# Optimization experiments

Measured on AMD Instinct MI355X. Metric: run time of the kernel, lower is better.

## Reference

```python
import jax, jax.numpy as jnp
import numpy as np

NC, L, C, V, H = 4, 3, 32, 512, 512
B, T, N = 32, 64, 8

def setup_inputs() -> dict:
    key = jax.random.key(0)
    ks = jax.random.split(key, 12)
    inp = {
        "x": jax.random.normal(ks[0], (B, T, N, H), dtype=jnp.float32),
        "comms": jax.random.randint(ks[1], (B, T, N, NC, L), 0, V, dtype=jnp.int64),
        "codebook": jax.random.normal(ks[2], (L, V, C), dtype=jnp.float32),
    }
    for l in range(L):
        fan_in = H + l * NC * C
        inp[f"W{l}"] = jax.random.normal(ks[3 + 2 * l], (NC * V, fan_in), dtype=jnp.float32) / np.sqrt(fan_in)
        inp[f"b{l}"] = jax.random.normal(ks[4 + 2 * l], (NC * V,), dtype=jnp.float32) * 0.01
    return inp


def reference(x, comms, codebook, W0, b0, W1, b1, W2, b2):
    # x: [B,T,N,H]; comms: [B,T,N,NC,L] int indices; codebook: [L,V,C]
    Bs, Ts, Ns, _ = x.shape
    params = [(W0, b0), (W1, b1), (W2, b2)]
    cond = x
    log_probs = jnp.zeros((Bs, Ts, Ns), dtype=x.dtype)
    entropy = jnp.zeros((Bs, Ts, Ns), dtype=x.dtype)
    hard_levels, soft_levels = [], []
    for l in range(L):
        W, b = params[l]
        logits = (cond @ W.T + b).reshape(Bs, Ts, Ns, NC, V)
        logp = jax.nn.log_softmax(logits, axis=-1)
        p = jnp.exp(logp)
        idx = comms[..., l]  # [B,T,N,NC]
        # log-prob of chosen codes, summed over comm channels
        lp = jnp.take_along_axis(logp, idx[..., None], axis=-1)[..., 0]
        log_probs = log_probs + lp.sum(axis=-1)
        # categorical entropy, summed over comm channels
        entropy = entropy + (-(p * logp).sum(axis=-1)).sum(axis=-1)
        hard = codebook[l][idx]                               # [B,T,N,NC,C]
        soft = jnp.einsum('btnkv,vc->btnkc', p, codebook[l])  # [B,T,N,NC,C]
        hard_levels.append(hard)
        soft_levels.append(soft)
        cond = jnp.concatenate([cond, hard.reshape(Bs, Ts, Ns, NC * C)], axis=-1)
    hard_s = jnp.stack(hard_levels, axis=-2)  # [B,T,N,NC,L,C]
    soft_s = jnp.stack(soft_levels, axis=-2)
    # straight-through estimator
    codewords = soft_s + jax.lax.stop_gradient(hard_s - soft_s)
    comm_output = codewords.sum(axis=-2).reshape(-1, NC * C)  # sum over hq levels
    return comm_output, log_probs, entropy
```

## Files before the change

kernel.cpp:

```cpp
#include <hip/hip_runtime.h>
#include <hip/hip_bf16.h>

#define NCC 4
#define LL 3
#define CCC 32
#define VVV 512
#define HHH 512
#define ROWS_TOTAL 16384
#define CONDW 768

typedef float f32x4 __attribute__((ext_vector_type(4)));
typedef long  i64f;
typedef long  i64x2 __attribute__((ext_vector_type(2)));

__device__ __forceinline__ void gload_lds16(const void* g, void* l) {
    __builtin_amdgcn_global_load_lds(
        (const __attribute__((address_space(1))) void*)g,
        (__attribute__((address_space(3))) void*)l, 16, 0, 0);
}

__device__ __forceinline__ int pk4_fp8(float a, float b, float c, float d) {
    int w = __builtin_amdgcn_cvt_pk_fp8_f32(a, b, 0, false);
    w = __builtin_amdgcn_cvt_pk_fp8_f32(c, d, w, true);
    return w;
}

__device__ __forceinline__ int perm_off(int b) {
    return (b & ~63) | ((b & 0x18) << 1) | ((b & 0x20) >> 2) | (b & 7);
}

__global__ void convert_w_fp8(const float* __restrict__ src, unsigned char* __restrict__ dst, int n) {
    int i = (blockIdx.x * blockDim.x + threadIdx.x) * 8;
    if (i + 7 < n) {
        const float4 v0 = *reinterpret_cast<const float4*>(src + i);
        const float4 v1 = *reinterpret_cast<const float4*>(src + i + 4);
        int2 p;
        p.x = pk4_fp8(v0.x, v0.y, v0.z, v0.w);
        p.y = pk4_fp8(v1.x, v1.y, v1.z, v1.w);
        *reinterpret_cast<int2*>(dst + perm_off(i)) = p;
    }
}

__global__ void build_cond(const float* __restrict__ x,
                           const int* __restrict__ comms,
                           const float* __restrict__ codebook,
                           unsigned char* __restrict__ cond,
                           float* __restrict__ comm_out) {
    const int r = blockIdx.x;
    const int t = threadIdx.x;
    const float4 v = reinterpret_cast<const float4*>(x + (size_t)r * HHH)[t];
    unsigned char* crow = cond + (size_t)r * CONDW;
    *reinterpret_cast<int*>(crow + perm_off(t * 4)) = pk4_fp8(v.x, v.y, v.z, v.w);
    const int k = t >> 5, c = t & 31;
    float s = 0.f;
    #pragma unroll
    for (int l = 0; l < LL; ++l) {
        const int vi = comms[r * (NCC * LL) + k * LL + l];
        const float val = codebook[((size_t)(l * VVV + vi)) * CCC + c];
        s += val;
        if (l < 2)
            crow[perm_off(HHH + l * (NCC * CCC) + t)] =
                (unsigned char)(__builtin_amdgcn_cvt_pk_fp8_f32(val, val, 0, false) & 0xff);
    }
    comm_out[(size_t)r * (NCC * CCC) + t] = s;
}

__global__ __launch_bounds__(256, 4) void gemm_partials(
    const unsigned char* __restrict__ cond,
    const unsigned char* __restrict__ wq,
    const float* __restrict__ b0, const float* __restrict__ b1, const float* __restrict__ b2,
    const int* __restrict__ comms,
    float4* __restrict__ partials)
{
    const int rb  = blockIdx.x;
    const int y   = blockIdx.y;
    const int lvl = blockIdx.z;
    const int K = HHH + lvl * (NCC * CCC);
    const unsigned char* W =
        wq + (lvl == 0 ? 0 : (lvl == 1 ? 2048 * 512 : 2048 * 512 + 2048 * 640));
    const float* bias = (lvl == 0) ? b0 : (lvl == 1 ? b1 : b2);

    const int tid  = threadIdx.x;
    const int lane = tid & 63;
    const int w    = tid >> 6;
    const int wr   = w >> 1;
    const int wc   = w & 1;
    const int lc   = lane & 15;
    const int kq   = lane >> 4;
    const int rchunk = (kq ^ ((lc >> 1) & 3)) << 4;

    const int rowBase = rb * 128;
    const int colBase = y * 128;

    __shared__ __align__(16) char LDS[32768];

    const int sc = (lane & 3) ^ ((lane >> 3) & 3);
    const unsigned char* gA = cond + (size_t)(rowBase + w * 32 + (lane >> 2)) * CONDW + sc * 16;
    const unsigned char* gB = W    + (size_t)(colBase + w * 32 + (lane >> 2)) * K     + sc * 16;

#define STAGE(B, KS) do {                                              \
        char* ab = LDS + (B) * 16384 + w * 2048;                       \
        gload_lds16(gA + (KS), ab);                                    \
        gload_lds16(gA + (size_t)16 * CONDW + (KS), ab + 1024);        \
        gload_lds16(gB + (KS), ab + 8192);                             \
        gload_lds16(gB + (size_t)16 * K + (KS), ab + 8192 + 1024);     \
    } while (0)

    f32x4 acc[4][4] = {};

    const int NT = K >> 6;
    STAGE(0, 0);
    asm volatile("s_waitcnt vmcnt(0)" ::: "memory");
    __builtin_amdgcn_s_barrier();

    for (int t = 0; t < NT; ++t) {
        const int cur = t & 1;
        if (t + 1 < NT) STAGE(cur ^ 1, (t + 1) * 64);
        const char* Ab = LDS + cur * 16384;
        const char* Bb = Ab + 8192;
        i64x2 af[4], bf[4];
        #pragma unroll
        for (int m = 0; m < 4; ++m)
            af[m] = *reinterpret_cast<const i64x2*>(
                Ab + (wr * 64 + m * 16 + lc) * 64 + rchunk);
        #pragma unroll
        for (int n = 0; n < 4; ++n)
            bf[n] = *reinterpret_cast<const i64x2*>(
                Bb + (wc * 64 + n * 16 + lc) * 64 + rchunk);
        __builtin_amdgcn_s_setprio(1);
        #pragma unroll
        for (int m = 0; m < 4; ++m)
            #pragma unroll
            for (int n = 0; n < 4; ++n)
                acc[m][n] = __builtin_amdgcn_mfma_f32_16x16x32_fp8_fp8(
                    af[m][0], bf[n][0], acc[m][n], 0, 0, 0);
        #pragma unroll
        for (int m = 0; m < 4; ++m)
            #pragma unroll
            for (int n = 0; n < 4; ++n)
                acc[m][n] = __builtin_amdgcn_mfma_f32_16x16x32_fp8_fp8(
                    af[m][1], bf[n][1], acc[m][n], 0, 0, 0);
        __builtin_amdgcn_s_setprio(0);
        asm volatile("s_waitcnt vmcnt(0)" ::: "memory");
        __builtin_amdgcn_s_barrier();
    }
#undef STAGE

    float* redS  = (float*)LDS;
    float* redT  = redS + 256;
    float* redTL = redT + 256;

    const int g   = y >> 2;
    const int cig = y & 3;
    float bv[4];
    #pragma unroll
    for (int n = 0; n < 4; ++n) bv[n] = bias[colBase + wc * 64 + n * 16 + lc];

    #pragma unroll
    for (int m = 0; m < 4; ++m) {
        float sv[4] = {0, 0, 0, 0}, tv[4] = {0, 0, 0, 0};
        #pragma unroll
        for (int i = 0; i < 4; ++i) {
            #pragma unroll
            for (int n = 0; n < 4; ++n) {
                const float z = acc[m][n][i] + bv[n];
                const float e = __expf(z);
                sv[i] += e;
                tv[i] += e * z;
            }
            #pragma unroll
            for (int off = 1; off < 16; off <<= 1) {
                sv[i] += __shfl_xor(sv[i], off);
                tv[i] += __shfl_xor(tv[i], off);
            }
        }
        #pragma unroll
        for (int i = 0; i < 4; ++i) {
            const int rloc = wr * 64 + m * 16 + kq * 4 + i;
            const int tcol = comms[(size_t)(rowBase + rloc) * (NCC * LL) + g * LL + lvl];
            #pragma unroll
            for (int n = 0; n < 4; ++n) {
                const int colg = cig * 128 + wc * 64 + n * 16 + lc;
                if (colg == tcol) redTL[rloc] = acc[m][n][i] + bv[n];
            }
        }
        if (lc == 0) {
            #pragma unroll
            for (int i = 0; i < 4; ++i) {
                const int rloc = wr * 64 + m * 16 + kq * 4 + i;
                redS[wc * 128 + rloc] = sv[i];
                redT[wc * 128 + rloc] = tv[i];
            }
        }
    }
    __syncthreads();
    if (tid < 128) {
        const int r = tid;
        const float S = redS[r] + redS[128 + r];
        const float T = redT[r] + redT[128 + r];
        partials[((size_t)lvl * ROWS_TOTAL + rowBase + r) * 16 + y] =
            make_float4(0.f, S, T, redTL[r]);
    }
}

__global__ void combine(const float4* __restrict__ partials,
                        const int* __restrict__ comms,
                        float* __restrict__ lp_out, float* __restrict__ ent_out)
{
    const int row = blockIdx.x * 256 + threadIdx.x;
    if (row >= ROWS_TOTAL) return;
    float lp = 0.f, ent = 0.f;
    #pragma unroll
    for (int lvl = 0; lvl < LL; ++lvl) {
        const float4* base = partials + ((size_t)lvl * ROWS_TOTAL + row) * 16;
        #pragma unroll
        for (int g = 0; g < NCC; ++g) {
            const int tcol = comms[(size_t)row * (NCC * LL) + g * LL + lvl];
            float S = 0.f, T = 0.f, tl = 0.f;
            #pragma unroll
            for (int k = 0; k < 4; ++k) {
                const float4 c = base[g * 4 + k];
                S += c.y;
                T += c.z;
                if ((tcol >> 7) == k) tl = c.w;
            }
            const float logZ = __logf(S);
            ent += logZ - T / S;
            lp += tl - logZ;
        }
    }
    lp_out[row] = lp;
    ent_out[row] = ent;
}

extern "C" void kernel_launch(void* const* d_in, const int* in_sizes, int n_in,
                              void* d_out, int out_size, void* d_ws, size_t ws_size,
                              hipStream_t stream) {
    const float* x        = (const float*)d_in[0];
    const int*   comms    = (const int*)d_in[1];
    const float* codebook = (const float*)d_in[2];
    const float* W0 = (const float*)d_in[3];
    const float* b0 = (const float*)d_in[4];
    const float* W1 = (const float*)d_in[5];
    const float* b1 = (const float*)d_in[6];
    const float* W2 = (const float*)d_in[7];
    const float* b2 = (const float*)d_in[8];

    float* out      = (float*)d_out;
    float* comm_out = out;
    float* lp_out   = out + (size_t)ROWS_TOTAL * 128;
    float* ent_out  = lp_out + ROWS_TOTAL;

    unsigned char* wq   = (unsigned char*)d_ws;
    unsigned char* cond = (unsigned char*)d_ws + 7864320;
    float4*       parts = (float4*)((char*)d_ws + 7864320 + 12582912);

    const int n0 = 2048 * 512, n1 = 2048 * 640, n2 = 2048 * 768;
    convert_w_fp8<<<n0 / 8 / 256, 256, 0, stream>>>(W0, wq, n0);
    convert_w_fp8<<<n1 / 8 / 256, 256, 0, stream>>>(W1, wq + n0, n1);
    convert_w_fp8<<<n2 / 8 / 256, 256, 0, stream>>>(W2, wq + n0 + n1, n2);

    build_cond<<<ROWS_TOTAL, 128, 0, stream>>>(x, comms, codebook, cond, comm_out);

    dim3 grid(ROWS_TOTAL / 128, 16, LL);
    gemm_partials<<<grid, 256, 0, stream>>>(cond, wq, b0, b1, b2, comms, parts);

    combine<<<ROWS_TOTAL / 256, 256, 0, stream>>>(parts, comms, lp_out, ent_out);
}
```

Baseline: 152.9 us.

## Pre-pack FP8 weights into MFMA fragment order and load B directly to registers

The weight conversion kernel now writes FP8 weights in a layout that matches the per-lane MFMA B-fragment order. The GEMM then loads B fragments straight from global memory into registers instead of staging them through LDS. This halves the LDS footprint, which may allow higher occupancy, and removes the LDS writes and reads for B. The cost is that each wave issues global loads for B directly, with cross-block reuse left to the cache. The global-load latency also sits inside the loop, since B is no longer prefetched a stage ahead.

Measured after the change: 145.8 us. 4.7% less time.

```diff
diff --git a/kernel.cpp b/kernel.cpp
--- a/kernel.cpp
+++ b/kernel.cpp
@@ -10,7 +10,6 @@
 #define CONDW 768
 
 typedef float f32x4 __attribute__((ext_vector_type(4)));
-typedef long  i64f;
 typedef long  i64x2 __attribute__((ext_vector_type(2)));
 
 __device__ __forceinline__ void gload_lds16(const void* g, void* l) {
@@ -29,16 +28,20 @@
     return (b & ~63) | ((b & 0x18) << 1) | ((b & 0x20) >> 2) | (b & 7);
 }
 
-__global__ void convert_w_fp8(const float* __restrict__ src, unsigned char* __restrict__ dst, int n) {
-    int i = (blockIdx.x * blockDim.x + threadIdx.x) * 8;
-    if (i + 7 < n) {
-        const float4 v0 = *reinterpret_cast<const float4*>(src + i);
-        const float4 v1 = *reinterpret_cast<const float4*>(src + i + 4);
-        int2 p;
-        p.x = pk4_fp8(v0.x, v0.y, v0.z, v0.w);
-        p.y = pk4_fp8(v1.x, v1.y, v1.z, v1.w);
-        *reinterpret_cast<int2*>(dst + perm_off(i)) = p;
-    }
+__global__ void convert_w_pack(const float* __restrict__ src, unsigned char* __restrict__ dst, int K) {
+    const int j  = blockIdx.x * 256 + threadIdx.x;
+    const int kc = K >> 3;
+    const int r  = j / kc;
+    const int k0 = (j - r * kc) * 8;
+    const float4 v0 = *reinterpret_cast<const float4*>(src + (size_t)r * K + k0);
+    const float4 v1 = *reinterpret_cast<const float4*>(src + (size_t)r * K + k0 + 4);
+    int2 p;
+    p.x = pk4_fp8(v0.x, v0.y, v0.z, v0.w);
+    p.y = pk4_fp8(v1.x, v1.y, v1.z, v1.w);
+    const int ct = r >> 4, lc = r & 15;
+    const int t = k0 >> 6, s = (k0 >> 5) & 1, kq = (k0 >> 3) & 3;
+    const size_t off = ((size_t)((t * 128 + ct) * 64 + kq * 16 + lc)) * 16 + s * 8;
+    *reinterpret_cast<int2*>(dst + off) = p;
 }
 
 __global__ void build_cond(const float* __restrict__ x,
@@ -76,7 +79,7 @@
     const int y   = blockIdx.y;
     const int lvl = blockIdx.z;
     const int K = HHH + lvl * (NCC * CCC);
-    const unsigned char* W =
+    const unsigned char* Wp =
         wq + (lvl == 0 ? 0 : (lvl == 1 ? 2048 * 512 : 2048 * 512 + 2048 * 640));
     const float* bias = (lvl == 0) ? b0 : (lvl == 1 ? b1 : b2);
 
@@ -90,43 +93,39 @@
     const int rchunk = (kq ^ ((lc >> 1) & 3)) << 4;
 
     const int rowBase = rb * 128;
-    const int colBase = y * 128;
-
-    __shared__ __align__(16) char LDS[32768];
+
+    __shared__ __align__(16) char LDS[16384];
 
     const int sc = (lane & 3) ^ ((lane >> 3) & 3);
     const unsigned char* gA = cond + (size_t)(rowBase + w * 32 + (lane >> 2)) * CONDW + sc * 16;
-    const unsigned char* gB = W    + (size_t)(colBase + w * 32 + (lane >> 2)) * K     + sc * 16;
-
-#define STAGE(B, KS) do {                                              \
-        char* ab = LDS + (B) * 16384 + w * 2048;                       \
+    const unsigned char* gBf = Wp + ((size_t)(y * 8 + wc * 4) * 64 + lane) * 16;
+
+#define STAGE_A(B, KS) do {                                            \
+        char* ab = LDS + (B) * 8192 + w * 2048;                        \
         gload_lds16(gA + (KS), ab);                                    \
         gload_lds16(gA + (size_t)16 * CONDW + (KS), ab + 1024);        \
-        gload_lds16(gB + (KS), ab + 8192);                             \
-        gload_lds16(gB + (size_t)16 * K + (KS), ab + 8192 + 1024);     \
     } while (0)
 
     f32x4 acc[4][4] = {};
 
     const int NT = K >> 6;
-    STAGE(0, 0);
+    STAGE_A(0, 0);
     asm volatile("s_waitcnt vmcnt(0)" ::: "memory");
     __builtin_amdgcn_s_barrier();
 
     for (int t = 0; t < NT; ++t) {
         const int cur = t & 1;
-        if (t + 1 < NT) STAGE(cur ^ 1, (t + 1) * 64);
-        const char* Ab = LDS + cur * 16384;
-        const char* Bb = Ab + 8192;
-        i64x2 af[4], bf[4];
+        i64x2 bf[4];
+        #pragma unroll
+        for (int n = 0; n < 4; ++n)
+            bf[n] = *reinterpret_cast<const i64x2*>(gBf + (size_t)t * 131072 + n * 1024);
+        if (t + 1 < NT) STAGE_A(cur ^ 1, (t + 1) * 64);
+        const char* Ab = LDS + cur * 8192;
+        i64x2 af[4];
         #pragma unroll
         for (int m = 0; m < 4; ++m)
             af[m] = *reinterpret_cast<const i64x2*>(
                 Ab + (wr * 64 + m * 16 + lc) * 64 + rchunk);
-        #pragma unroll
-        for (int n = 0; n < 4; ++n)
-            bf[n] = *reinterpret_cast<const i64x2*>(
-                Bb + (wc * 64 + n * 16 + lc) * 64 + rchunk);
         __builtin_amdgcn_s_setprio(1);
         #pragma unroll
         for (int m = 0; m < 4; ++m)
@@ -144,7 +143,7 @@
         asm volatile("s_waitcnt vmcnt(0)" ::: "memory");
         __builtin_amdgcn_s_barrier();
     }
-#undef STAGE
+#undef STAGE_A
 
     float* redS  = (float*)LDS;
     float* redT  = redS + 256;
@@ -152,6 +151,7 @@
 
     const int g   = y >> 2;
     const int cig = y & 3;
+    const int colBase = y * 128;
     float bv[4];
     #pragma unroll
     for (int n = 0; n < 4; ++n) bv[n] = bias[colBase + wc * 64 + n * 16 + lc];
@@ -256,9 +256,9 @@
     float4*       parts = (float4*)((char*)d_ws + 7864320 + 12582912);
 
     const int n0 = 2048 * 512, n1 = 2048 * 640, n2 = 2048 * 768;
-    convert_w_fp8<<<n0 / 8 / 256, 256, 0, stream>>>(W0, wq, n0);
-    convert_w_fp8<<<n1 / 8 / 256, 256, 0, stream>>>(W1, wq + n0, n1);
-    convert_w_fp8<<<n2 / 8 / 256, 256, 0, stream>>>(W2, wq + n0 + n1, n2);
+    convert_w_pack<<<512, 256, 0, stream>>>(W0, wq, 512);
+    convert_w_pack<<<640, 256, 0, stream>>>(W1, wq + n0, 640);
+    convert_w_pack<<<768, 256, 0, stream>>>(W2, wq + n0 + n1, 768);
 
     build_cond<<<ROWS_TOTAL, 128, 0, stream>>>(x, comms, codebook, cond, comm_out);
 
```
